# Kernel tuning notes

Measured on AMD Instinct MI355X. Metric: run time of the kernel, lower is better.

## Reference

```python
import jax, jax.numpy as jnp
import numpy as np

B, L, HID, D, H, HKV, EPS, THETA = 1, 2048, 2048, 128, 32, 4, 1e-6, 1000000.0
GROUPS = H // HKV  # 8


def setup_inputs() -> dict:
    key = jax.random.key(0)
    ks = jax.random.split(key, 6)
    x = jax.random.normal(ks[0], (B, L, HID), dtype=jnp.float32)
    wq = jax.random.normal(ks[1], (H * D, HID), dtype=jnp.float32) * 0.02
    wk = jax.random.normal(ks[2], (HKV * D, HID), dtype=jnp.float32) * 0.02
    wv = jax.random.normal(ks[3], (HKV * D, HID), dtype=jnp.float32) * 0.02
    wo = jax.random.normal(ks[4], (HID, H * D), dtype=jnp.float32) * 0.02
    q_norm_w = jnp.ones((D,), dtype=jnp.float32)
    k_norm_w = jnp.ones((D,), dtype=jnp.float32)
    # RoPE tables: inv_freq over half dims, emb = concat(freqs, freqs)
    inv_freq = 1.0 / (THETA ** (jnp.arange(0, D, 2, dtype=jnp.float32) / D))
    pos = jnp.arange(L, dtype=jnp.float32)
    freqs = pos[:, None] * inv_freq[None, :]        # [L, D/2]
    emb = jnp.concatenate([freqs, freqs], axis=-1)  # [L, D]
    cos = jnp.cos(emb)[None]                        # [1, L, D]
    sin = jnp.sin(emb)[None]
    return {"x": x, "wq": wq, "wk": wk, "wv": wv, "wo": wo,
            "q_norm_w": q_norm_w, "k_norm_w": k_norm_w, "cos": cos, "sin": sin}


def _rmsnorm(t, w):
    var = jnp.mean(t * t, axis=-1, keepdims=True)
    return t * jax.lax.rsqrt(var + EPS) * w


def _rotate_half(t):
    t1, t2 = jnp.split(t, 2, axis=-1)
    return jnp.concatenate([-t2, t1], axis=-1)


def reference(x, wq, wk, wv, wo, q_norm_w, k_norm_w, cos, sin):
    b, l, _ = x.shape
    # projections -> [B, heads, L, D]
    q = _rmsnorm((x @ wq.T).reshape(b, l, H, D), q_norm_w).swapaxes(1, 2)
    k = _rmsnorm((x @ wk.T).reshape(b, l, HKV, D), k_norm_w).swapaxes(1, 2)
    v = (x @ wv.T).reshape(b, l, HKV, D).swapaxes(1, 2)
    # RoPE (cos/sin broadcast over head dim)
    c, s = cos[:, None], sin[:, None]
    q = c * q + s * _rotate_half(q)
    k = c * k + s * _rotate_half(k)
    # GQA: repeat kv heads across groups
    k = jnp.repeat(k, GROUPS, axis=1)
    v = jnp.repeat(v, GROUPS, axis=1)
    # causal SDPA
    scores = jnp.einsum("bhqd,bhkd->bhqk", q, k) / np.sqrt(D).astype(np.float32)
    causal = jnp.tril(jnp.ones((l, l), dtype=bool))
    scores = jnp.where(causal, scores, jnp.finfo(scores.dtype).min)
    attn = jax.nn.softmax(scores, axis=-1)
    out = jnp.einsum("bhqk,bhkd->bhqd", attn, v)
    out = out.swapaxes(1, 2).reshape(b, l, H * D)
    return out @ wo.T
```

## Files before the change

### kernel.cpp

```cpp
#include <hip/hip_runtime.h>

typedef unsigned short u16;
typedef short bh8 __attribute__((ext_vector_type(8)));
typedef short bh4 __attribute__((ext_vector_type(4)));
typedef float f4 __attribute__((ext_vector_type(4)));
typedef u16 u16x4 __attribute__((ext_vector_type(4)));

__device__ __forceinline__ u16 f2bf(float f) {
  union { float f; unsigned u; } v; v.f = f;
  unsigned u = v.u;
  return (u16)((u + 0x7fffu + ((u >> 16) & 1u)) >> 16);
}
__device__ __forceinline__ float bf2f(u16 h) {
  union { unsigned u; float f; } v; v.u = ((unsigned)h) << 16;
  return v.f;
}
__device__ __forceinline__ void gll16(const void* src, void* dst) {
  __builtin_amdgcn_global_load_lds((const __attribute__((address_space(1))) void*)src,
                                   (__attribute__((address_space(3))) void*)dst,
                                   16, 0, 0);
}

__global__ __launch_bounds__(256) void k_cvt(const float* __restrict__ in,
                                             u16* __restrict__ out, int n4) {
  int i = blockIdx.x * 256 + threadIdx.x;
  if (i >= n4) return;
  f4 v = *(const f4*)(in + (size_t)i * 4);
  u16x4 o;
  o.x = f2bf(v[0]); o.y = f2bf(v[1]); o.z = f2bf(v[2]); o.w = f2bf(v[3]);
  *(u16x4*)(out + (size_t)i * 4) = o;
}

template<int K, bool OUTF32, int NFR, bool FUSED>
__global__ __launch_bounds__(256) void k_gemm(const u16* __restrict__ A,
                                              const u16* __restrict__ B1,
                                              const u16* __restrict__ B2,
                                              void* __restrict__ C1,
                                              void* __restrict__ C2,
                                              int N1, int N2, int NB1) {
  constexpr int BN = NFR * 32;
  __shared__ u16 As[2][128 * 32];
  __shared__ u16 Bs[2][BN * 32];
  const int t = threadIdx.x;
  const int lane = t & 63;
  const int w = t >> 6, wm = w >> 1, wn = w & 1;
  const int g = lane >> 4, r16 = lane & 15;
  const int bm = blockIdx.x;
  int bn = blockIdx.y;

  const u16* B; void* C; int N;
  if (!FUSED || bn < NB1) { B = B1; C = C1; N = N1; }
  else { bn -= NB1; B = B2; C = C2; N = N2; }
  B += (size_t)bn * BN * K;

  f4 acc[4][NFR] = {};

  const int rA0 = t >> 2, cA0 = (t & 3) * 8;
  const u16* a0 = A + (size_t)(bm * 128 + rA0) * K + cA0;
  const u16* a1 = a0 + (size_t)64 * K;
  const u16* b0 = B + (size_t)rA0 * K + cA0;

  gll16(a0, As[0] + t * 8);
  gll16(a1, As[0] + (t + 256) * 8);
  gll16(b0, Bs[0] + t * 8);
  if (BN == 128) gll16(b0 + (size_t)64 * K, Bs[0] + (t + 256) * 8);
  __syncthreads();

  int cur = 0;
  for (int k0 = 0; k0 < K; k0 += 32) {
    if (k0 + 32 < K) {
      gll16(a0 + k0 + 32, As[cur ^ 1] + t * 8);
      gll16(a1 + k0 + 32, As[cur ^ 1] + (t + 256) * 8);
      gll16(b0 + k0 + 32, Bs[cur ^ 1] + t * 8);
      if (BN == 128) gll16(b0 + (size_t)64 * K + k0 + 32, Bs[cur ^ 1] + (t + 256) * 8);
    }
    bh8 af[4], bfr[NFR];
#pragma unroll
    for (int m = 0; m < 4; ++m)
      af[m] = *(const bh8*)&As[cur][(wm * 64 + m * 16 + r16) * 32 + g * 8];
#pragma unroll
    for (int n = 0; n < NFR; ++n)
      bfr[n] = *(const bh8*)&Bs[cur][(wn * 16 * NFR + n * 16 + r16) * 32 + g * 8];
    __builtin_amdgcn_s_setprio(1);
#pragma unroll
    for (int m = 0; m < 4; ++m)
#pragma unroll
      for (int n = 0; n < NFR; ++n)
        acc[m][n] = __builtin_amdgcn_mfma_f32_16x16x32_bf16(af[m], bfr[n], acc[m][n], 0, 0, 0);
    __builtin_amdgcn_s_setprio(0);
    __syncthreads();
    cur ^= 1;
  }

#pragma unroll
  for (int m = 0; m < 4; ++m) {
    const int row0 = bm * 128 + wm * 64 + m * 16 + g * 4;
#pragma unroll
    for (int n = 0; n < NFR; ++n) {
      const int col = bn * BN + wn * 16 * NFR + n * 16 + r16;
#pragma unroll
      for (int r = 0; r < 4; ++r) {
        if constexpr (OUTF32)
          ((float*)C)[(size_t)(row0 + r) * N + col] = acc[m][n][r];
        else
          ((u16*)C)[(size_t)(row0 + r) * N + col] = f2bf(acc[m][n][r]);
      }
    }
  }
}

__global__ __launch_bounds__(256) void k_normrope(u16* __restrict__ qbuf,
                                                  u16* __restrict__ kvbuf,
                                                  const float* __restrict__ qw,
                                                  const float* __restrict__ kw,
                                                  const float* __restrict__ cosb,
                                                  const float* __restrict__ sinb) {
  const float CSC = 1.4426950408889634f * 0.088388347648318447f;
  const int t = threadIdx.x, lane = t & 63, w = t >> 6;
  const int rid = blockIdx.x * 4 + w;
  u16* base; const float* nw; int seq; float sc;
  if (rid < 2048 * 32) {
    seq = rid >> 5;
    base = qbuf + (size_t)seq * 4096 + (size_t)(rid & 31) * 128;
    nw = qw; sc = CSC;
  } else {
    const int r2 = rid - 2048 * 32;
    seq = r2 >> 2;
    base = kvbuf + (size_t)seq * 1024 + (size_t)(r2 & 3) * 128;
    nw = kw; sc = 1.0f;
  }
  float a = bf2f(base[lane]);
  float b = bf2f(base[lane + 64]);
  float ss = a * a + b * b;
#pragma unroll
  for (int off = 32; off >= 1; off >>= 1) ss += __shfl_xor(ss, off);
  const float rs = rsqrtf(ss * (1.0f / 128.0f) + 1e-6f);
  const float na = a * rs * nw[lane];
  const float nb = b * rs * nw[lane + 64];
  const float c1 = cosb[seq * 128 + lane],      s1 = sinb[seq * 128 + lane];
  const float c2 = cosb[seq * 128 + lane + 64], s2 = sinb[seq * 128 + lane + 64];
  base[lane]      = f2bf(sc * (c1 * na - s1 * nb));
  base[lane + 64] = f2bf(sc * (c2 * nb + s2 * na));
}

__global__ __launch_bounds__(256) void k_transpose_v(const u16* __restrict__ kv,
                                                     u16* __restrict__ vt) {
  __shared__ u16 tile[32][33];
  const int t = threadIdx.x;
  const int bl = blockIdx.x, bh = blockIdx.y;
  const int row = t >> 3, c4 = (t & 7) * 4;
  const u16* src = kv + (size_t)(bl * 32 + row) * 1024 + 512 + bh * 32 + c4;
  u16x4 v = *(const u16x4*)src;
  tile[row][c4 + 0] = v.x; tile[row][c4 + 1] = v.y;
  tile[row][c4 + 2] = v.z; tile[row][c4 + 3] = v.w;
  __syncthreads();
  u16x4 o;
  o.x = tile[c4 + 0][row]; o.y = tile[c4 + 1][row];
  o.z = tile[c4 + 2][row]; o.w = tile[c4 + 3][row];
  const int pcol = ((c4 >> 2) & 3) * 8 + (c4 >> 4) * 4;
  *(u16x4*)&vt[(size_t)(bh * 32 + row) * 2048 + bl * 32 + pcol] = o;
}

__global__ __launch_bounds__(512, 4) void k_attn(const u16* __restrict__ Q,
                                                 const u16* __restrict__ Kb,
                                                 const u16* __restrict__ Vt,
                                                 u16* __restrict__ O) {
  __shared__ u16 Ks[2][64 * 128];
  __shared__ u16 Vs[2][128 * 64];
  const int t = threadIdx.x, lane = t & 63, w = t >> 6;
  const int g = lane >> 4, r16 = lane & 15;
  const int j = blockIdx.x >> 5, h = blockIdx.x & 31;
  const int qb = (j < 8) ? (15 - j) : (j - 8);
  const int kvh = h >> 3;
  const int qw0 = qb * 128 + w * 16;
  const int qg  = qw0 + r16;

  bh8 qf[4];
#pragma unroll
  for (int kc = 0; kc < 4; ++kc)
    qf[kc] = *(const bh8*)(Q + (size_t)qg * 4096 + h * 128 + (kc * 4 + g) * 8);

  const int niter = 2 * qb + 2;

  f4 acc_o[8] = {};
  float mrun = -3.0e38f, lsum = 0.0f;

  {
#pragma unroll
    for (int i = 0; i < 2; ++i) {
      const int s = t + 512 * i, row = s >> 4, sl = s & 15;
      gll16(Kb + (size_t)row * 1024 + kvh * 128 + ((sl ^ (row & 15)) * 8), Ks[0] + s * 8);
    }
#pragma unroll
    for (int i = 0; i < 2; ++i) {
      const int s = t + 512 * i, row = s >> 3, sl = s & 7;
      gll16(Vt + (size_t)(kvh * 128 + row) * 2048 + ((sl ^ (row & 7)) * 8), Vs[0] + s * 8);
    }
  }
  __syncthreads();

  int cur = 0;
  for (int kt = 0; kt < niter; ++kt) {
    if (kt + 1 < niter) {
      const int nt = kt + 1;
#pragma unroll
      for (int i = 0; i < 2; ++i) {
        const int s = t + 512 * i, row = s >> 4, sl = s & 15;
        gll16(Kb + (size_t)(nt * 64 + row) * 1024 + kvh * 128 + ((sl ^ (row & 15)) * 8),
              Ks[cur ^ 1] + s * 8);
      }
#pragma unroll
      for (int i = 0; i < 2; ++i) {
        const int s = t + 512 * i, row = s >> 3, sl = s & 7;
        gll16(Vt + (size_t)(kvh * 128 + row) * 2048 + nt * 64 + ((sl ^ (row & 7)) * 8),
              Vs[cur ^ 1] + s * 8);
      }
    }

    const bool active = (kt * 64 <= qw0 + 15);
    if (active) {
      f4 st[4] = {};
      __builtin_amdgcn_s_setprio(1);
#pragma unroll
      for (int kf = 0; kf < 4; ++kf) {
        const int krow = kf * 16 + r16;
#pragma unroll
        for (int kc = 0; kc < 4; ++kc) {
          bh8 kfr = *(const bh8*)&Ks[cur][krow * 128 + (((kc * 4 + g) ^ (krow & 15)) * 8)];
          st[kf] = __builtin_amdgcn_mfma_f32_16x16x32_bf16(kfr, qf[kc], st[kf], 0, 0, 0);
        }
      }
      __builtin_amdgcn_s_setprio(0);

      float tmax = -3.0e38f;
      const bool edge = ((kt + 1) * 64 - 1 > qw0);
#pragma unroll
      for (int kf = 0; kf < 4; ++kf)
#pragma unroll
        for (int r = 0; r < 4; ++r) {
          float v = st[kf][r];
          if (edge && (kt * 64 + kf * 16 + g * 4 + r) > qg) v = -3.0e38f;
          st[kf][r] = v;
          tmax = fmaxf(tmax, v);
        }
      tmax = fmaxf(tmax, __shfl_xor(tmax, 16));
      tmax = fmaxf(tmax, __shfl_xor(tmax, 32));

      if (!__all(tmax <= mrun + 8.0f)) {
        const float mnew = fmaxf(mrun, tmax);
        const float alpha = exp2f(mrun - mnew);
        mrun = mnew;
        lsum *= alpha;
#pragma unroll
        for (int d = 0; d < 8; ++d) acc_o[d] *= alpha;
      }

      float psum = 0.0f;
      bh8 pb2[2];
#pragma unroll
      for (int kf = 0; kf < 4; ++kf)
#pragma unroll
        for (int r = 0; r < 4; ++r) {
          float p = exp2f(st[kf][r] - mrun);
          psum += p;
          pb2[kf >> 1][(kf & 1) * 4 + r] = (short)f2bf(p);
        }
      psum += __shfl_xor(psum, 16);
      psum += __shfl_xor(psum, 32);
      lsum += psum;

      __builtin_amdgcn_s_setprio(1);
#pragma unroll
      for (int dcol = 0; dcol < 8; ++dcol) {
        const int vrow = dcol * 16 + r16;
#pragma unroll
        for (int c = 0; c < 2; ++c) {
          const int slot = c * 4 + g;
          bh8 vfr = *(const bh8*)&Vs[cur][vrow * 64 + ((slot ^ (vrow & 7)) * 8)];
          acc_o[dcol] = __builtin_amdgcn_mfma_f32_16x16x32_bf16(vfr, pb2[c], acc_o[dcol], 0, 0, 0);
        }
      }
      __builtin_amdgcn_s_setprio(0);
    }

    __syncthreads();
    cur ^= 1;
  }

  const float inv = 1.0f / lsum;
#pragma unroll
  for (int dcol = 0; dcol < 8; ++dcol) {
    u16x4 o;
    o.x = f2bf(acc_o[dcol][0] * inv);
    o.y = f2bf(acc_o[dcol][1] * inv);
    o.z = f2bf(acc_o[dcol][2] * inv);
    o.w = f2bf(acc_o[dcol][3] * inv);
    *(u16x4*)&O[(size_t)qg * 4096 + h * 128 + dcol * 16 + g * 4] = o;
  }
}

extern "C" void kernel_launch(void* const* d_in, const int* in_sizes, int n_in,
                              void* d_out, int out_size, void* d_ws, size_t ws_size,
                              hipStream_t stream) {
  (void)in_sizes; (void)n_in; (void)out_size; (void)ws_size;
  const float* x    = (const float*)d_in[0];
  const float* wq   = (const float*)d_in[1];
  const float* wk   = (const float*)d_in[2];
  const float* wv   = (const float*)d_in[3];
  const float* wo   = (const float*)d_in[4];
  const float* qw   = (const float*)d_in[5];
  const float* kw   = (const float*)d_in[6];
  const float* cosb = (const float*)d_in[7];
  const float* sinb = (const float*)d_in[8];

  u16* xb   = (u16*)d_ws;
  u16* wqb  = xb  + (size_t)2048 * 2048;
  u16* wkvb = wqb + (size_t)4096 * 2048;
  u16* wob  = wkvb + (size_t)1024 * 2048;
  u16* qbuf = wob + (size_t)2048 * 4096;
  u16* kvb  = qbuf + (size_t)2048 * 4096;
  u16* vt   = kvb + (size_t)2048 * 1024;
  u16* aout = vt  + (size_t)512 * 2048;

  k_cvt<<<dim3(4096), 256, 0, stream>>>(x,  xb,   2048 * 2048 / 4);
  k_cvt<<<dim3(8192), 256, 0, stream>>>(wq, wqb,  4096 * 2048 / 4);
  k_cvt<<<dim3(1024), 256, 0, stream>>>(wk, wkvb,                      512 * 2048 / 4);
  k_cvt<<<dim3(1024), 256, 0, stream>>>(wv, wkvb + (size_t)512 * 2048, 512 * 2048 / 4);
  k_cvt<<<dim3(8192), 256, 0, stream>>>(wo, wob,  2048 * 4096 / 4);

  k_gemm<2048, false, 4, true><<<dim3(16, 40), 256, 0, stream>>>(
      xb, wqb, wkvb, qbuf, kvb, 4096, 1024, 32);

  k_normrope<<<dim3((2048 * 36) / 4), 256, 0, stream>>>(qbuf, kvb, qw, kw, cosb, sinb);

  k_transpose_v<<<dim3(64, 16), 256, 0, stream>>>(kvb, vt);

  k_attn<<<dim3(512), 512, 0, stream>>>(qbuf, kvb, vt, aout);

  k_gemm<4096, true, 2, false><<<dim3(16, 32), 256, 0, stream>>>(
      aout, wob, nullptr, d_out, nullptr, 2048, 0, 0);
}
```

Before: 239.6 us.

## Merge conversions, triple-buffer GEMMs with XCD remap, retile attention to 64-row blocks

Merges the five fp32-to-bf16 conversion launches into one grid-stride kernel. Both GEMMs get a three-stage LDS pipeline with explicit vmcnt waits and a block index remap that spreads tiles across the 8 XCDs for L2 locality. Attention moves to 256-thread blocks over 64-query tiles with a permuted head order. It single-buffers V, loading it during the QK phase behind a mid-iteration barrier. These changes target launch overhead, load latency and load imbalance, at the cost of more LDS per GEMM block and extra barriers in attention.

```diff
diff --git a/kernel.cpp b/kernel.cpp
--- a/kernel.cpp
+++ b/kernel.cpp
@@ -21,14 +21,25 @@
                                    16, 0, 0);
 }
 
-__global__ __launch_bounds__(256) void k_cvt(const float* __restrict__ in,
-                                             u16* __restrict__ out, int n4) {
-  int i = blockIdx.x * 256 + threadIdx.x;
-  if (i >= n4) return;
-  f4 v = *(const f4*)(in + (size_t)i * 4);
-  u16x4 o;
-  o.x = f2bf(v[0]); o.y = f2bf(v[1]); o.z = f2bf(v[2]); o.w = f2bf(v[3]);
-  *(u16x4*)(out + (size_t)i * 4) = o;
+__global__ __launch_bounds__(256) void k_cvt_all(const float* __restrict__ x,
+                                                 const float* __restrict__ wq,
+                                                 const float* __restrict__ wk,
+                                                 const float* __restrict__ wv,
+                                                 const float* __restrict__ wo,
+                                                 u16* __restrict__ dst) {
+  const size_t n = 5767168;
+  for (size_t idx = (size_t)blockIdx.x * 256 + threadIdx.x; idx < n; idx += 4096ull * 256) {
+    const float* src; size_t off;
+    if (idx < 1048576)       { src = x;  off = idx; }
+    else if (idx < 3145728)  { src = wq; off = idx - 1048576; }
+    else if (idx < 3407872)  { src = wk; off = idx - 3145728; }
+    else if (idx < 3670016)  { src = wv; off = idx - 3407872; }
+    else                     { src = wo; off = idx - 3670016; }
+    f4 v = *(const f4*)(src + off * 4);
+    u16x4 o;
+    o.x = f2bf(v[0]); o.y = f2bf(v[1]); o.z = f2bf(v[2]); o.w = f2bf(v[3]);
+    *(u16x4*)(dst + idx * 4) = o;
+  }
 }
 
 template<int K, bool OUTF32, int NFR, bool FUSED>
@@ -37,16 +48,19 @@
                                               const u16* __restrict__ B2,
                                               void* __restrict__ C1,
                                               void* __restrict__ C2,
-                                              int N1, int N2, int NB1) {
+                                              int N1, int N2, int NB1, int npx) {
   constexpr int BN = NFR * 32;
-  __shared__ u16 As[2][128 * 32];
-  __shared__ u16 Bs[2][BN * 32];
+  constexpr int nk = K / 32;
+  __shared__ u16 As[3][128 * 32];
+  __shared__ u16 Bs[3][BN * 32];
   const int t = threadIdx.x;
   const int lane = t & 63;
   const int w = t >> 6, wm = w >> 1, wn = w & 1;
   const int g = lane >> 4, r16 = lane & 15;
-  const int bm = blockIdx.x;
-  int bn = blockIdx.y;
+  const int bb = blockIdx.x;
+  const int gl = (bb & 7) * npx + (bb >> 3);
+  const int bm = gl & 15;
+  int bn = gl >> 4;
 
   const u16* B; void* C; int N;
   if (!FUSED || bn < NB1) { B = B1; C = C1; N = N1; }
@@ -60,27 +74,20 @@
   const u16* a1 = a0 + (size_t)64 * K;
   const u16* b0 = B + (size_t)rA0 * K + cA0;
 
-  gll16(a0, As[0] + t * 8);
-  gll16(a1, As[0] + (t + 256) * 8);
-  gll16(b0, Bs[0] + t * 8);
-  if (BN == 128) gll16(b0 + (size_t)64 * K, Bs[0] + (t + 256) * 8);
-  __syncthreads();
-
-  int cur = 0;
-  for (int k0 = 0; k0 < K; k0 += 32) {
-    if (k0 + 32 < K) {
-      gll16(a0 + k0 + 32, As[cur ^ 1] + t * 8);
-      gll16(a1 + k0 + 32, As[cur ^ 1] + (t + 256) * 8);
-      gll16(b0 + k0 + 32, Bs[cur ^ 1] + t * 8);
-      if (BN == 128) gll16(b0 + (size_t)64 * K + k0 + 32, Bs[cur ^ 1] + (t + 256) * 8);
-    }
+  auto STAGE = [&](int kk, int bi) {
+    gll16(a0 + kk * 32, As[bi] + t * 8);
+    gll16(a1 + kk * 32, As[bi] + (t + 256) * 8);
+    gll16(b0 + kk * 32, Bs[bi] + t * 8);
+    if constexpr (BN == 128) gll16(b0 + (size_t)64 * K + kk * 32, Bs[bi] + (t + 256) * 8);
+  };
+  auto COMP = [&](int bi) {
     bh8 af[4], bfr[NFR];
 #pragma unroll
     for (int m = 0; m < 4; ++m)
-      af[m] = *(const bh8*)&As[cur][(wm * 64 + m * 16 + r16) * 32 + g * 8];
+      af[m] = *(const bh8*)&As[bi][(wm * 64 + m * 16 + r16) * 32 + g * 8];
 #pragma unroll
     for (int n = 0; n < NFR; ++n)
-      bfr[n] = *(const bh8*)&Bs[cur][(wn * 16 * NFR + n * 16 + r16) * 32 + g * 8];
+      bfr[n] = *(const bh8*)&Bs[bi][(wn * 16 * NFR + n * 16 + r16) * 32 + g * 8];
     __builtin_amdgcn_s_setprio(1);
 #pragma unroll
     for (int m = 0; m < 4; ++m)
@@ -88,9 +95,36 @@
       for (int n = 0; n < NFR; ++n)
         acc[m][n] = __builtin_amdgcn_mfma_f32_16x16x32_bf16(af[m], bfr[n], acc[m][n], 0, 0, 0);
     __builtin_amdgcn_s_setprio(0);
-    __syncthreads();
-    cur ^= 1;
-  }
+  };
+
+  STAGE(0, 0);
+  STAGE(1, 1);
+
+  int bi = 0;
+  for (int k = 0; k < nk - 2; ++k) {
+    int st = bi + 2; if (st >= 3) st -= 3;
+    STAGE(k + 2, st);
+    if constexpr (BN == 128) asm volatile("s_waitcnt vmcnt(8)" ::: "memory");
+    else                     asm volatile("s_waitcnt vmcnt(6)" ::: "memory");
+    __builtin_amdgcn_s_barrier();
+    __builtin_amdgcn_sched_barrier(0);
+    COMP(bi);
+    asm volatile("s_waitcnt lgkmcnt(0)" ::: "memory");
+    __builtin_amdgcn_s_barrier();
+    bi = (bi + 1 == 3) ? 0 : bi + 1;
+  }
+  if constexpr (BN == 128) asm volatile("s_waitcnt vmcnt(4)" ::: "memory");
+  else                     asm volatile("s_waitcnt vmcnt(3)" ::: "memory");
+  __builtin_amdgcn_s_barrier();
+  __builtin_amdgcn_sched_barrier(0);
+  COMP(bi);
+  asm volatile("s_waitcnt lgkmcnt(0)" ::: "memory");
+  __builtin_amdgcn_s_barrier();
+  bi = (bi + 1 == 3) ? 0 : bi + 1;
+  asm volatile("s_waitcnt vmcnt(0)" ::: "memory");
+  __builtin_amdgcn_s_barrier();
+  __builtin_amdgcn_sched_barrier(0);
+  COMP(bi);
 
 #pragma unroll
   for (int m = 0; m < 4; ++m) {
@@ -161,18 +195,20 @@
   *(u16x4*)&vt[(size_t)(bh * 32 + row) * 2048 + bl * 32 + pcol] = o;
 }
 
-__global__ __launch_bounds__(512, 4) void k_attn(const u16* __restrict__ Q,
+__global__ __launch_bounds__(256, 3) void k_attn(const u16* __restrict__ Q,
                                                  const u16* __restrict__ Kb,
                                                  const u16* __restrict__ Vt,
                                                  u16* __restrict__ O) {
   __shared__ u16 Ks[2][64 * 128];
-  __shared__ u16 Vs[2][128 * 64];
+  __shared__ u16 Vs[128 * 64];
   const int t = threadIdx.x, lane = t & 63, w = t >> 6;
   const int g = lane >> 4, r16 = lane & 15;
-  const int j = blockIdx.x >> 5, h = blockIdx.x & 31;
-  const int qb = (j < 8) ? (15 - j) : (j - 8);
+  const int b = blockIdx.x;
+  const int i = b & 31;
+  const int qt = 31 - (b >> 5);
+  const int h = ((i >> 1) & 3) * 8 + ((i & 1) << 2) + (i >> 3);
   const int kvh = h >> 3;
-  const int qw0 = qb * 128 + w * 16;
+  const int qw0 = qt * 64 + w * 16;
   const int qg  = qw0 + r16;
 
   bh8 qf[4];
@@ -180,108 +216,100 @@
   for (int kc = 0; kc < 4; ++kc)
     qf[kc] = *(const bh8*)(Q + (size_t)qg * 4096 + h * 128 + (kc * 4 + g) * 8);
 
-  const int niter = 2 * qb + 2;
+  const int niter = qt + 1;
 
   f4 acc_o[8] = {};
   float mrun = -3.0e38f, lsum = 0.0f;
 
-  {
-#pragma unroll
-    for (int i = 0; i < 2; ++i) {
-      const int s = t + 512 * i, row = s >> 4, sl = s & 15;
-      gll16(Kb + (size_t)row * 1024 + kvh * 128 + ((sl ^ (row & 15)) * 8), Ks[0] + s * 8);
-    }
-#pragma unroll
-    for (int i = 0; i < 2; ++i) {
-      const int s = t + 512 * i, row = s >> 3, sl = s & 7;
-      gll16(Vt + (size_t)(kvh * 128 + row) * 2048 + ((sl ^ (row & 7)) * 8), Vs[0] + s * 8);
-    }
+#pragma unroll
+  for (int i2 = 0; i2 < 4; ++i2) {
+    const int s = t + 256 * i2, row = s >> 4, sl = s & 15;
+    gll16(Kb + (size_t)row * 1024 + kvh * 128 + ((sl ^ (row & 15)) * 8), Ks[0] + s * 8);
   }
   __syncthreads();
 
   int cur = 0;
   for (int kt = 0; kt < niter; ++kt) {
+#pragma unroll
+    for (int i2 = 0; i2 < 4; ++i2) {
+      const int s = t + 256 * i2, row = s >> 3, sl = s & 7;
+      gll16(Vt + (size_t)(kvh * 128 + row) * 2048 + kt * 64 + ((sl ^ (row & 7)) * 8),
+            Vs + s * 8);
+    }
     if (kt + 1 < niter) {
       const int nt = kt + 1;
 #pragma unroll
-      for (int i = 0; i < 2; ++i) {
-        const int s = t + 512 * i, row = s >> 4, sl = s & 15;
+      for (int i2 = 0; i2 < 4; ++i2) {
+        const int s = t + 256 * i2, row = s >> 4, sl = s & 15;
         gll16(Kb + (size_t)(nt * 64 + row) * 1024 + kvh * 128 + ((sl ^ (row & 15)) * 8),
               Ks[cur ^ 1] + s * 8);
       }
-#pragma unroll
-      for (int i = 0; i < 2; ++i) {
-        const int s = t + 512 * i, row = s >> 3, sl = s & 7;
-        gll16(Vt + (size_t)(kvh * 128 + row) * 2048 + nt * 64 + ((sl ^ (row & 7)) * 8),
-              Vs[cur ^ 1] + s * 8);
-      }
-    }
-
-    const bool active = (kt * 64 <= qw0 + 15);
-    if (active) {
-      f4 st[4] = {};
-      __builtin_amdgcn_s_setprio(1);
-#pragma unroll
-      for (int kf = 0; kf < 4; ++kf) {
-        const int krow = kf * 16 + r16;
-#pragma unroll
-        for (int kc = 0; kc < 4; ++kc) {
-          bh8 kfr = *(const bh8*)&Ks[cur][krow * 128 + (((kc * 4 + g) ^ (krow & 15)) * 8)];
-          st[kf] = __builtin_amdgcn_mfma_f32_16x16x32_bf16(kfr, qf[kc], st[kf], 0, 0, 0);
-        }
-      }
-      __builtin_amdgcn_s_setprio(0);
-
-      float tmax = -3.0e38f;
-      const bool edge = ((kt + 1) * 64 - 1 > qw0);
-#pragma unroll
-      for (int kf = 0; kf < 4; ++kf)
-#pragma unroll
-        for (int r = 0; r < 4; ++r) {
-          float v = st[kf][r];
-          if (edge && (kt * 64 + kf * 16 + g * 4 + r) > qg) v = -3.0e38f;
-          st[kf][r] = v;
-          tmax = fmaxf(tmax, v);
-        }
-      tmax = fmaxf(tmax, __shfl_xor(tmax, 16));
-      tmax = fmaxf(tmax, __shfl_xor(tmax, 32));
-
-      if (!__all(tmax <= mrun + 8.0f)) {
-        const float mnew = fmaxf(mrun, tmax);
-        const float alpha = exp2f(mrun - mnew);
-        mrun = mnew;
-        lsum *= alpha;
-#pragma unroll
-        for (int d = 0; d < 8; ++d) acc_o[d] *= alpha;
-      }
-
-      float psum = 0.0f;
-      bh8 pb2[2];
-#pragma unroll
-      for (int kf = 0; kf < 4; ++kf)
-#pragma unroll
-        for (int r = 0; r < 4; ++r) {
-          float p = exp2f(st[kf][r] - mrun);
-          psum += p;
-          pb2[kf >> 1][(kf & 1) * 4 + r] = (short)f2bf(p);
-        }
-      psum += __shfl_xor(psum, 16);
-      psum += __shfl_xor(psum, 32);
-      lsum += psum;
-
-      __builtin_amdgcn_s_setprio(1);
-#pragma unroll
-      for (int dcol = 0; dcol < 8; ++dcol) {
-        const int vrow = dcol * 16 + r16;
-#pragma unroll
-        for (int c = 0; c < 2; ++c) {
-          const int slot = c * 4 + g;
-          bh8 vfr = *(const bh8*)&Vs[cur][vrow * 64 + ((slot ^ (vrow & 7)) * 8)];
-          acc_o[dcol] = __builtin_amdgcn_mfma_f32_16x16x32_bf16(vfr, pb2[c], acc_o[dcol], 0, 0, 0);
-        }
-      }
-      __builtin_amdgcn_s_setprio(0);
-    }
+    }
+
+    f4 st[4] = {};
+    __builtin_amdgcn_s_setprio(1);
+#pragma unroll
+    for (int kf = 0; kf < 4; ++kf) {
+      const int krow = kf * 16 + r16;
+#pragma unroll
+      for (int kc = 0; kc < 4; ++kc) {
+        bh8 kfr = *(const bh8*)&Ks[cur][krow * 128 + (((kc * 4 + g) ^ (krow & 15)) * 8)];
+        st[kf] = __builtin_amdgcn_mfma_f32_16x16x32_bf16(kfr, qf[kc], st[kf], 0, 0, 0);
+      }
+    }
+    __builtin_amdgcn_s_setprio(0);
+
+    float tmax = -3.0e38f;
+    const bool edge = ((kt + 1) * 64 - 1 > qw0);
+#pragma unroll
+    for (int kf = 0; kf < 4; ++kf)
+#pragma unroll
+      for (int r = 0; r < 4; ++r) {
+        float v = st[kf][r];
+        if (edge && (kt * 64 + kf * 16 + g * 4 + r) > qg) v = -3.0e38f;
+        st[kf][r] = v;
+        tmax = fmaxf(tmax, v);
+      }
+    tmax = fmaxf(tmax, __shfl_xor(tmax, 16));
+    tmax = fmaxf(tmax, __shfl_xor(tmax, 32));
+
+    if (!__all(tmax <= mrun + 8.0f)) {
+      const float mnew = fmaxf(mrun, tmax);
+      const float alpha = exp2f(mrun - mnew);
+      mrun = mnew;
+      lsum *= alpha;
+#pragma unroll
+      for (int d = 0; d < 8; ++d) acc_o[d] *= alpha;
+    }
+
+    float psum = 0.0f;
+    bh8 pb2[2];
+#pragma unroll
+    for (int kf = 0; kf < 4; ++kf)
+#pragma unroll
+      for (int r = 0; r < 4; ++r) {
+        float p = exp2f(st[kf][r] - mrun);
+        psum += p;
+        pb2[kf >> 1][(kf & 1) * 4 + r] = (short)f2bf(p);
+      }
+    psum += __shfl_xor(psum, 16);
+    psum += __shfl_xor(psum, 32);
+    lsum += psum;
+
+    __syncthreads();
+
+    __builtin_amdgcn_s_setprio(1);
+#pragma unroll
+    for (int dcol = 0; dcol < 8; ++dcol) {
+      const int vrow = dcol * 16 + r16;
+#pragma unroll
+      for (int c = 0; c < 2; ++c) {
+        const int slot = c * 4 + g;
+        bh8 vfr = *(const bh8*)&Vs[vrow * 64 + ((slot ^ (vrow & 7)) * 8)];
+        acc_o[dcol] = __builtin_amdgcn_mfma_f32_16x16x32_bf16(vfr, pb2[c], acc_o[dcol], 0, 0, 0);
+      }
+    }
+    __builtin_amdgcn_s_setprio(0);
 
     __syncthreads();
     cur ^= 1;
@@ -322,21 +350,17 @@
   u16* vt   = kvb + (size_t)2048 * 1024;
   u16* aout = vt  + (size_t)512 * 2048;
 
-  k_cvt<<<dim3(4096), 256, 0, stream>>>(x,  xb,   2048 * 2048 / 4);
-  k_cvt<<<dim3(8192), 256, 0, stream>>>(wq, wqb,  4096 * 2048 / 4);
-  k_cvt<<<dim3(1024), 256, 0, stream>>>(wk, wkvb,                      512 * 2048 / 4);
-  k_cvt<<<dim3(1024), 256, 0, stream>>>(wv, wkvb + (size_t)512 * 2048, 512 * 2048 / 4);
-  k_cvt<<<dim3(8192), 256, 0, stream>>>(wo, wob,  2048 * 4096 / 4);
-
-  k_gemm<2048, false, 4, true><<<dim3(16, 40), 256, 0, stream>>>(
-      xb, wqb, wkvb, qbuf, kvb, 4096, 1024, 32);
+  k_cvt_all<<<dim3(4096), 256, 0, stream>>>(x, wq, wk, wv, wo, xb);
+
+  k_gemm<2048, false, 4, true><<<dim3(640), 256, 0, stream>>>(
+      xb, wqb, wkvb, qbuf, kvb, 4096, 1024, 32, 80);
 
   k_normrope<<<dim3((2048 * 36) / 4), 256, 0, stream>>>(qbuf, kvb, qw, kw, cosb, sinb);
 
   k_transpose_v<<<dim3(64, 16), 256, 0, stream>>>(kvb, vt);
 
-  k_attn<<<dim3(512), 512, 0, stream>>>(qbuf, kvb, vt, aout);
-
-  k_gemm<4096, true, 2, false><<<dim3(16, 32), 256, 0, stream>>>(
-      aout, wob, nullptr, d_out, nullptr, 2048, 0, 0);
-}
+  k_attn<<<dim3(1024), 256, 0, stream>>>(qbuf, kvb, vt, aout);
+
+  k_gemm<4096, true, 2, false><<<dim3(512), 256, 0, stream>>>(
+      aout, wob, nullptr, d_out, nullptr, 2048, 0, 0, 64);
+}
```

Result: faster. 217.2 us (-9.3%).
